# Performance work log

Hardware: AMD Instinct MI355X
Metric: run time of the kernel (lower is better)

The kernel has to match this reference:

```python
import jax, jax.numpy as jnp
import numpy as np

M = 70  # SDP matrix size (hardcoded in source)
N = 85  # number of constraints (hardcoded in source)


def setup_inputs() -> dict:
    key = jax.random.key(0)
    ks = jax.random.split(key, 6)
    return {
        "rho1": jax.random.normal(ks[0], (70, 70), jnp.float32),
        "mu1": jax.random.normal(ks[1], (85, 1), jnp.float32),
        "v1": jax.random.normal(ks[2], (4, 1), jnp.float32),
        "t": jax.random.normal(ks[3], (4, 1), jnp.float32),
        "H1": jax.random.normal(ks[4], (8, 8), jnp.float32),
        "c": jax.random.uniform(ks[5], (1,), jnp.float32),
    }


def reference(rho1, mu1, v1, t, H1, c):
    dt = H1.dtype
    gamma1 = 0.1            # 1/gamma, gamma = 10
    Q = 400.0               # (1/epsilon)^2, epsilon = 0.05
    sigma2 = 4e-4           # sigma^2, sigma = 0.02

    H = 0.2 * H1
    h111, h112, h121, h122 = H[:, 0], H[:, 2], H[:, 5], H[:, 7]
    z8 = jnp.zeros(8, dt)
    I8 = jnp.eye(8, dtype=dt)

    def uv(off, corner, h):
        # u_i = e_{off+i} + h[i] * e_corner, stacked over i -> [8, M]
        U = jnp.zeros((8, M), dt).at[jnp.arange(8), off + jnp.arange(8)].set(1.0)
        return U.at[:, corner].add(h)

    # shared (i==i) term: entries (68,69) and (69,68)
    D6869 = jnp.zeros((M, M), dt).at[68, 69].set(1.0).at[69, 68].set(1.0)
    diag_term = jnp.einsum('ij,mn->ijmn', I8, D6869)

    # A[i,j] = sum_b coeff_b * outer(u_i^b, u_j^b)  (+ diag term for i==j)
    UA = jnp.stack([uv(0, 8, h111), uv(9, 17, h112), uv(18, 26, h121),
                    uv(27, 35, h122), uv(36, 8, z8)])
    cA = jnp.array([gamma1, -1.0, -1.0, -1.0, 1.0], dt)
    A = jnp.einsum('b,bim,bjn->ijmn', cA, UA, UA) + diag_term

    UB = jnp.stack([uv(0, 8, h111), uv(9, 17, h112), uv(18, 26, h121),
                    uv(27, 35, h122), uv(44, 8, z8)])
    cB = jnp.array([-1.0, gamma1, -1.0, -1.0, 1.0], dt)
    B = jnp.einsum('b,bim,bjn->ijmn', cB, UB, UB) + diag_term

    # symmetric vectorization over upper triangle: k-th = A[i,j]+A[j,i] (i<j), A[i,i] on diag
    ii, jj = np.triu_indices(8)
    scale = jnp.asarray(np.where(ii == jj, 0.5, 1.0), dt)[:, None, None]
    Asvec = (A + A.transpose(1, 0, 2, 3))[ii, jj] * scale   # [36, M, M]
    Bsvec = (B + B.transpose(1, 0, 2, 3))[ii, jj] * scale   # [36, M, M]

    A2 = jnp.zeros((13, M, M), dt)
    A2 = A2.at[0, 0:8, 0:8].set(Q * I8).at[0, 8, 8].set(-1.0).at[0, 52, 52].set(1.0)
    A2 = A2.at[1, 9:17, 9:17].set(Q * I8).at[1, 17, 17].set(-1.0).at[1, 53, 53].set(1.0)
    A2 = A2.at[2, 18:26, 18:26].set(Q * I8).at[2, 26, 26].set(-1.0).at[2, 54, 54].set(1.0)
    A2 = A2.at[3, 27:35, 27:35].set(Q * I8).at[3, 35, 35].set(-1.0).at[3, 55, 55].set(1.0)
    A2 = A2.at[4, 8, 8].set(-1.0).at[4, 56, 56].set(1.0).at[4, 60, 61].set(1.0).at[4, 61, 60].set(1.0)
    A2 = A2.at[5, 17, 17].set(-1.0).at[5, 57, 57].set(1.0).at[5, 62, 63].set(1.0).at[5, 63, 62].set(1.0)
    A2 = A2.at[6, 26, 26].set(1.0).at[6, 58, 58].set(1.0).at[6, 64, 65].set(1.0).at[6, 65, 64].set(1.0)
    A2 = A2.at[7, 35, 35].set(1.0).at[7, 59, 59].set(1.0).at[7, 66, 67].set(1.0).at[7, 67, 66].set(1.0)
    A2 = A2.at[8, 60, 60].set(1.0).at[9, 62, 62].set(1.0).at[10, 64, 64].set(1.0)
    A2 = A2.at[11, 66, 66].set(1.0).at[12, 68, 68].set(1.0)

    ones_idx = np.array([0, 8, 15, 21, 26, 30, 33, 35])
    b = jnp.zeros((N, 1), dt)
    b = b.at[ones_idx, 0].set(1.0).at[ones_idx + 36, 0].set(1.0)
    b = b.at[76:80, 0].set(v1[:, 0])
    b = b.at[80:85, 0].set(c[0] * 0.5)

    A0 = jnp.zeros((M, M), dt)
    A0 = A0.at[8, 8].set(-sigma2).at[17, 17].set(-sigma2)
    d_idx = jnp.array([61, 63, 65, 67, 69])
    A0 = A0.at[d_idx, d_idx].set(1.0)
    rows = jnp.array([60, 62, 64, 66])
    cols = rows + 1
    tv = t[:, 0][jnp.array([2, 3, 0, 1])]  # t2, t3, t0, t1
    A0 = A0.at[rows, cols].set(tv).at[cols, rows].set(tv)

    AA = -jnp.concatenate([Asvec, Bsvec, A2], axis=0)  # [85, M, M]
    return AA, -b, A0
```

## Files before the change

### kernel.cpp

```cpp
#include <hip/hip_runtime.h>


#define MDIM 70
#define AA_ELEMS (85 * MDIM * MDIM)
#define B_OFF    AA_ELEMS
#define A0_OFF   (AA_ELEMS + 85)
#define TOT      (AA_ELEMS + 85 + MDIM * MDIM)

__global__ __launch_bounds__(256) void z1_fill_kernel(
    const float* __restrict__ v1,
    const float* __restrict__ t,
    const float* __restrict__ H1,
    const float* __restrict__ c,
    float* __restrict__ out)
{
    int idx = blockIdx.x * blockDim.x + threadIdx.x;
    if (idx >= TOT) return;

    if (idx < AA_ELEMS) {
        int k = idx / (MDIM * MDIM);
        int r = idx - k * (MDIM * MDIM);
        int m = r / MDIM;
        int n = r - m * MDIM;

        float val;
        if (k < 72) {
            const bool isB = (k >= 36);
            int kk = isB ? (k - 36) : k;
            int i = 0;
            while (kk >= 8 - i) { kk -= 8 - i; ++i; }
            int j = i + kk;

            float hi0 = 0.2f * H1[i * 8 + 0];
            float hi1 = 0.2f * H1[i * 8 + 2];
            float hi2 = 0.2f * H1[i * 8 + 5];
            float hi3 = 0.2f * H1[i * 8 + 7];
            float hj0 = 0.2f * H1[j * 8 + 0];
            float hj1 = 0.2f * H1[j * 8 + 2];
            float hj2 = 0.2f * H1[j * 8 + 5];
            float hj3 = 0.2f * H1[j * 8 + 7];

            float hiv[4] = {hi0, hi1, hi2, hi3};
            float hjv[4] = {hj0, hj1, hj2, hj3};

            float aij = 0.0f, aji = 0.0f;
            #pragma unroll
            for (int b = 0; b < 4; ++b) {
                float cb = (!isB ? (b == 0) : (b == 1)) ? 0.1f : -1.0f;
                int off = 9 * b;
                int cor = 9 * b + 8;
                float uim = (m == off + i ? 1.0f : 0.0f) + (m == cor ? hiv[b] : 0.0f);
                float ujn = (n == off + j ? 1.0f : 0.0f) + (n == cor ? hjv[b] : 0.0f);
                float ujm = (m == off + j ? 1.0f : 0.0f) + (m == cor ? hjv[b] : 0.0f);
                float uin = (n == off + i ? 1.0f : 0.0f) + (n == cor ? hiv[b] : 0.0f);
                aij += cb * uim * ujn;
                aji += cb * ujm * uin;
            }
            int base4 = isB ? 44 : 36;
            if (m == base4 + i && n == base4 + j) aij += 1.0f;
            if (m == base4 + j && n == base4 + i) aji += 1.0f;
            if (i == j && ((m == 68 && n == 69) || (m == 69 && n == 68))) {
                aij += 1.0f;
                aji += 1.0f;
            }
            float s = (i == j) ? 0.5f : 1.0f;
            val = (aij + aji) * s;
        } else {
            int k2 = k - 72;
            float v = 0.0f;
            if (k2 < 4) {
                int lo = 9 * k2;
                if (m == n) {
                    if (m >= lo && m < lo + 8)      v = 400.0f;
                    else if (m == lo + 8)           v = -1.0f;
                    else if (m == 52 + k2)          v = 1.0f;
                }
            } else if (k2 < 8) {
                int q = k2 - 4;
                int cpos = 9 * q + 8;
                float csgn = (q < 2) ? -1.0f : 1.0f;
                if (m == n) {
                    if (m == cpos)          v = csgn;
                    else if (m == 56 + q)   v = 1.0f;
                } else {
                    int base = 60 + 2 * q;
                    if ((m == base && n == base + 1) || (m == base + 1 && n == base))
                        v = 1.0f;
                }
            } else if (k2 < 12) {
                int p = 60 + 2 * (k2 - 8);
                if (m == p && n == p) v = 1.0f;
            } else {
                if (m == 68 && n == 68) v = 1.0f;
            }
            val = v;
        }
        out[idx] = -val;
    } else if (idx < A0_OFF) {
        int p = idx - B_OFF;
        float bv = 0.0f;
        bool one = (p == 0 || p == 8 || p == 15 || p == 21 ||
                    p == 26 || p == 30 || p == 33 || p == 35 ||
                    p == 36 || p == 44 || p == 51 || p == 57 ||
                    p == 62 || p == 66 || p == 69 || p == 71);
        if (one)                      bv = 1.0f;
        else if (p >= 76 && p < 80)   bv = v1[p - 76];
        else if (p >= 80)             bv = 0.5f * c[0];
        out[idx] = -bv;
    } else {
        int r = idx - A0_OFF;
        int m = r / MDIM;
        int n = r - m * MDIM;
        float v = 0.0f;
        if (m == n) {
            if (m == 8 || m == 17)                                   v = -0.0004f;
            else if (m == 61 || m == 63 || m == 65 || m == 67 || m == 69) v = 1.0f;
        } else {
            int lo = m < n ? m : n;
            int hi = m < n ? n : m;
            if (hi == lo + 1 && lo >= 60 && lo <= 66 && ((lo & 1) == 0)) {
                int q = (lo - 60) >> 1;
                v = t[q ^ 2];
            }
        }
        out[idx] = v;
    }
}

extern "C" void kernel_launch(void* const* d_in, const int* in_sizes, int n_in,
                              void* d_out, int out_size, void* d_ws, size_t ws_size,
                              hipStream_t stream) {
    const float* v1 = (const float*)d_in[2];
    const float* t  = (const float*)d_in[3];
    const float* H1 = (const float*)d_in[4];
    const float* c  = (const float*)d_in[5];
    float* out = (float*)d_out;

    const int threads = 256;
    const int blocks = (TOT + threads - 1) / threads;
    z1_fill_kernel<<<blocks, threads, 0, stream>>>(v1, t, H1, c, out);
}
```

Measured before the change: 9.854 us.

## Zero-fill slices with float4 stores then scatter only the sparse nonzeros

```diff
diff --git a/kernel.cpp b/kernel.cpp
--- a/kernel.cpp
+++ b/kernel.cpp
@@ -1,129 +1,128 @@
 #include <hip/hip_runtime.h>
 
 
-#define MDIM 70
-#define AA_ELEMS (85 * MDIM * MDIM)
+#define MDIM   70
+#define SLICE  (MDIM * MDIM)
+#define AA_ELEMS (85 * SLICE)
 #define B_OFF    AA_ELEMS
 #define A0_OFF   (AA_ELEMS + 85)
-#define TOT      (AA_ELEMS + 85 + MDIM * MDIM)
+#define TOT      (A0_OFF + SLICE)
 
-__global__ __launch_bounds__(256) void z1_fill_kernel(
+__constant__ int c_ones[16] = {0,8,15,21,26,30,33,35,36,44,51,57,62,66,69,71};
+__constant__ int c_diag[7]  = {8,17,61,63,65,67,69};
+
+__device__ __forceinline__ int candf(int sel, int i, int j, int base4) {
+    if (sel < 12) {
+        int b = (sel * 11) >> 5;
+        int r = sel - 3 * b;
+        return 9 * b + (r == 0 ? i : (r == 1 ? j : 8));
+    }
+    if (sel == 12) return base4 + i;
+    if (sel == 13) return base4 + j;
+    return 54 + sel;
+}
+
+__global__ __launch_bounds__(512) void z1_sparse_kernel(
     const float* __restrict__ v1,
     const float* __restrict__ t,
     const float* __restrict__ H1,
     const float* __restrict__ c,
     float* __restrict__ out)
 {
-    int idx = blockIdx.x * blockDim.x + threadIdx.x;
-    if (idx >= TOT) return;
+    const int k   = blockIdx.x;
+    const int tid = threadIdx.x;
 
-    if (idx < AA_ELEMS) {
-        int k = idx / (MDIM * MDIM);
-        int r = idx - k * (MDIM * MDIM);
-        int m = r / MDIM;
-        int n = r - m * MDIM;
+    if (k < 85) {
+        float4* base = (float4*)(out + k * SLICE);
+        for (int ch = tid; ch < 1225; ch += 512)
+            base[ch] = make_float4(0.f, 0.f, 0.f, 0.f);
+    } else {
+        float4* base = (float4*)(out + B_OFF);
+        for (int ch = tid; ch < 1246; ch += 512)
+            base[ch] = make_float4(0.f, 0.f, 0.f, 0.f);
+        if (tid == 0) out[TOT - 1] = 1.0f;
+    }
+    __syncthreads();
 
-        float val;
-        if (k < 72) {
-            const bool isB = (k >= 36);
-            int kk = isB ? (k - 36) : k;
-            int i = 0;
-            while (kk >= 8 - i) { kk -= 8 - i; ++i; }
-            int j = i + kk;
+    if (k < 72) {
+        if (tid >= 256) return;
+        const bool isB = (k >= 36);
+        int kk = isB ? (k - 36) : k;
+        int i = 0;
+        while (kk >= 8 - i) { kk -= 8 - i; ++i; }
+        const int j = i + kk;
+        const int base4 = isB ? 44 : 36;
 
-            float hi0 = 0.2f * H1[i * 8 + 0];
-            float hi1 = 0.2f * H1[i * 8 + 2];
-            float hi2 = 0.2f * H1[i * 8 + 5];
-            float hi3 = 0.2f * H1[i * 8 + 7];
-            float hj0 = 0.2f * H1[j * 8 + 0];
-            float hj1 = 0.2f * H1[j * 8 + 2];
-            float hj2 = 0.2f * H1[j * 8 + 5];
-            float hj3 = 0.2f * H1[j * 8 + 7];
+        const int m = candf(tid >> 4, i, j, base4);
+        const int n = candf(tid & 15, i, j, base4);
 
-            float hiv[4] = {hi0, hi1, hi2, hi3};
-            float hjv[4] = {hj0, hj1, hj2, hj3};
+        float hiv[4], hjv[4];
+        hiv[0] = 0.2f * H1[i * 8 + 0];  hjv[0] = 0.2f * H1[j * 8 + 0];
+        hiv[1] = 0.2f * H1[i * 8 + 2];  hjv[1] = 0.2f * H1[j * 8 + 2];
+        hiv[2] = 0.2f * H1[i * 8 + 5];  hjv[2] = 0.2f * H1[j * 8 + 5];
+        hiv[3] = 0.2f * H1[i * 8 + 7];  hjv[3] = 0.2f * H1[j * 8 + 7];
 
-            float aij = 0.0f, aji = 0.0f;
-            #pragma unroll
-            for (int b = 0; b < 4; ++b) {
-                float cb = (!isB ? (b == 0) : (b == 1)) ? 0.1f : -1.0f;
-                int off = 9 * b;
-                int cor = 9 * b + 8;
-                float uim = (m == off + i ? 1.0f : 0.0f) + (m == cor ? hiv[b] : 0.0f);
-                float ujn = (n == off + j ? 1.0f : 0.0f) + (n == cor ? hjv[b] : 0.0f);
-                float ujm = (m == off + j ? 1.0f : 0.0f) + (m == cor ? hjv[b] : 0.0f);
-                float uin = (n == off + i ? 1.0f : 0.0f) + (n == cor ? hiv[b] : 0.0f);
-                aij += cb * uim * ujn;
-                aji += cb * ujm * uin;
-            }
-            int base4 = isB ? 44 : 36;
-            if (m == base4 + i && n == base4 + j) aij += 1.0f;
-            if (m == base4 + j && n == base4 + i) aji += 1.0f;
-            if (i == j && ((m == 68 && n == 69) || (m == 69 && n == 68))) {
-                aij += 1.0f;
-                aji += 1.0f;
-            }
-            float s = (i == j) ? 0.5f : 1.0f;
-            val = (aij + aji) * s;
+        float aij = 0.0f, aji = 0.0f;
+        #pragma unroll
+        for (int b = 0; b < 4; ++b) {
+            float cb = (!isB ? (b == 0) : (b == 1)) ? 0.1f : -1.0f;
+            int off = 9 * b;
+            int cor = 9 * b + 8;
+            float uim = (m == off + i ? 1.0f : 0.0f) + (m == cor ? hiv[b] : 0.0f);
+            float ujn = (n == off + j ? 1.0f : 0.0f) + (n == cor ? hjv[b] : 0.0f);
+            float ujm = (m == off + j ? 1.0f : 0.0f) + (m == cor ? hjv[b] : 0.0f);
+            float uin = (n == off + i ? 1.0f : 0.0f) + (n == cor ? hiv[b] : 0.0f);
+            aij += cb * uim * ujn;
+            aji += cb * ujm * uin;
+        }
+        if (m == base4 + i && n == base4 + j) aij += 1.0f;
+        if (m == base4 + j && n == base4 + i) aji += 1.0f;
+        if (i == j && ((m == 68 && n == 69) || (m == 69 && n == 68))) {
+            aij += 1.0f;  aji += 1.0f;
+        }
+        const float s = (i == j) ? 0.5f : 1.0f;
+        out[k * SLICE + m * MDIM + n] = -((aij + aji) * s);
+    } else if (k < 85) {
+        const int k2 = k - 72;
+        const int bse = k * SLICE;
+        if (k2 < 4) {
+            const int lo = 9 * k2;
+            if (tid < 8)       out[bse + (lo + tid) * 71] = -400.0f;
+            else if (tid == 8) out[bse + (lo + 8) * 71]   =  1.0f;
+            else if (tid == 9) out[bse + (52 + k2) * 71]  = -1.0f;
+        } else if (k2 < 8) {
+            const int q = k2 - 4;
+            const int cpos = 9 * q + 8;
+            const int bb = 60 + 2 * q;
+            const float csgn = (q < 2) ? -1.0f : 1.0f;
+            if (tid == 0)      out[bse + cpos * 71]          = -csgn;
+            else if (tid == 1) out[bse + (56 + q) * 71]      = -1.0f;
+            else if (tid == 2) out[bse + bb * MDIM + bb + 1] = -1.0f;
+            else if (tid == 3) out[bse + (bb + 1) * MDIM + bb] = -1.0f;
+        } else if (k2 < 12) {
+            const int p = 60 + 2 * (k2 - 8);
+            if (tid == 0) out[bse + p * 71] = -1.0f;
         } else {
-            int k2 = k - 72;
-            float v = 0.0f;
-            if (k2 < 4) {
-                int lo = 9 * k2;
-                if (m == n) {
-                    if (m >= lo && m < lo + 8)      v = 400.0f;
-                    else if (m == lo + 8)           v = -1.0f;
-                    else if (m == 52 + k2)          v = 1.0f;
-                }
-            } else if (k2 < 8) {
-                int q = k2 - 4;
-                int cpos = 9 * q + 8;
-                float csgn = (q < 2) ? -1.0f : 1.0f;
-                if (m == n) {
-                    if (m == cpos)          v = csgn;
-                    else if (m == 56 + q)   v = 1.0f;
-                } else {
-                    int base = 60 + 2 * q;
-                    if ((m == base && n == base + 1) || (m == base + 1 && n == base))
-                        v = 1.0f;
-                }
-            } else if (k2 < 12) {
-                int p = 60 + 2 * (k2 - 8);
-                if (m == p && n == p) v = 1.0f;
-            } else {
-                if (m == 68 && n == 68) v = 1.0f;
-            }
-            val = v;
+            if (tid == 0) out[bse + 68 * 71] = -1.0f;
         }
-        out[idx] = -val;
-    } else if (idx < A0_OFF) {
-        int p = idx - B_OFF;
-        float bv = 0.0f;
-        bool one = (p == 0 || p == 8 || p == 15 || p == 21 ||
-                    p == 26 || p == 30 || p == 33 || p == 35 ||
-                    p == 36 || p == 44 || p == 51 || p == 57 ||
-                    p == 62 || p == 66 || p == 69 || p == 71);
-        if (one)                      bv = 1.0f;
-        else if (p >= 76 && p < 80)   bv = v1[p - 76];
-        else if (p >= 80)             bv = 0.5f * c[0];
-        out[idx] = -bv;
     } else {
-        int r = idx - A0_OFF;
-        int m = r / MDIM;
-        int n = r - m * MDIM;
-        float v = 0.0f;
-        if (m == n) {
-            if (m == 8 || m == 17)                                   v = -0.0004f;
-            else if (m == 61 || m == 63 || m == 65 || m == 67 || m == 69) v = 1.0f;
-        } else {
-            int lo = m < n ? m : n;
-            int hi = m < n ? n : m;
-            if (hi == lo + 1 && lo >= 60 && lo <= 66 && ((lo & 1) == 0)) {
-                int q = (lo - 60) >> 1;
-                v = t[q ^ 2];
-            }
+        if (tid < 16) {
+            out[B_OFF + c_ones[tid]] = -1.0f;
+        } else if (tid < 20) {
+            out[B_OFF + 76 + (tid - 16)] = -v1[tid - 16];
+        } else if (tid < 25) {
+            out[B_OFF + 80 + (tid - 20)] = -0.5f * c[0];
+        } else if (tid < 32) {
+            const int p = c_diag[tid - 25];
+            out[A0_OFF + p * 71] = (p == 8 || p == 17) ? -0.0004f : 1.0f;
+        } else if (tid < 40) {
+            const int e = tid - 32;
+            const int q = e >> 1;
+            const int row = 60 + 2 * q, col = row + 1;
+            const float tv = t[q ^ 2];
+            if (e & 1) out[A0_OFF + col * MDIM + row] = tv;
+            else       out[A0_OFF + row * MDIM + col] = tv;
         }
-        out[idx] = v;
     }
 }
 
@@ -136,7 +135,5 @@
     const float* c  = (const float*)d_in[5];
     float* out = (float*)d_out;
 
-    const int threads = 256;
-    const int blocks = (TOT + threads - 1) / threads;
-    z1_fill_kernel<<<blocks, threads, 0, stream>>>(v1, t, H1, c, out);
+    z1_sparse_kernel<<<86, 512, 0, stream>>>(v1, t, H1, c, out);
 }
```

Result: no change. 9.879 us (+0.3%).
